# Kernel tuning notes

Measured on AMD Instinct MI355X. Metric: run time of the kernel, lower is better.

Reference implementation:

```python
import jax, jax.numpy as jnp
import numpy as np

E = 12      # embed dim
H = 32      # MLP hidden
EPS = 1e-5  # LayerNorm eps


def _layer_norm(x, gamma, beta):
    mu = jnp.mean(x, axis=-1, keepdims=True)
    var = jnp.mean(jnp.square(x - mu), axis=-1, keepdims=True)
    return (x - mu) * jax.lax.rsqrt(var + EPS) * gamma + beta


def setup_inputs() -> dict:
    key = jax.random.key(0)
    ks = jax.random.split(key, 16)
    L, N = 128, 4096
    s = 1.0 / np.sqrt(E)
    inp = {
        "x": jax.random.normal(ks[0], (L, N, E), dtype=jnp.float32),
        # MultiheadAttention packed in-projection [3E, E] and bias [3E]
        "in_proj_w": jax.random.uniform(ks[1], (3 * E, E), minval=-s, maxval=s, dtype=jnp.float32),
        "in_proj_b": jnp.zeros((3 * E,), dtype=jnp.float32),
        "out_w": jax.random.uniform(ks[2], (E, E), minval=-s, maxval=s, dtype=jnp.float32),
        "out_b": jnp.zeros((E,), dtype=jnp.float32),
        # MLP: Linear(12,32) Tanh Linear(32,32) Tanh Linear(32,12) Tanh
        "w1": jax.random.uniform(ks[3], (H, E), minval=-s, maxval=s, dtype=jnp.float32),
        "b1": jnp.zeros((H,), dtype=jnp.float32),
        "w2": jax.random.uniform(ks[4], (H, H), minval=-1/np.sqrt(H), maxval=1/np.sqrt(H), dtype=jnp.float32),
        "b2": jnp.zeros((H,), dtype=jnp.float32),
        "w3": jax.random.uniform(ks[5], (E, H), minval=-1/np.sqrt(H), maxval=1/np.sqrt(H), dtype=jnp.float32),
        "b3": jnp.zeros((E,), dtype=jnp.float32),
        # LayerNorm affine params
        "g1": jnp.ones((E,), dtype=jnp.float32),
        "be1": jnp.zeros((E,), dtype=jnp.float32),
        "g2": jnp.ones((E,), dtype=jnp.float32),
        "be2": jnp.zeros((E,), dtype=jnp.float32),
    }
    return inp


def reference(x, in_proj_w, in_proj_b, out_w, out_b,
              w1, b1, w2, b2, w3, b3, g1, be1, g2, be2):
    # x: [L, N, E] (seq, batch, embed) -- torch MHA default layout
    # --- single-head self-attention ---
    qkv = jnp.einsum('lne,fe->lnf', x, in_proj_w) + in_proj_b  # [L, N, 3E]
    q, k, v = jnp.split(qkv, 3, axis=-1)
    scale = 1.0 / jnp.sqrt(jnp.asarray(E, x.dtype))
    scores = jnp.einsum('lne,mne->nlm', q * scale, k)          # [N, L, L]
    p = jax.nn.softmax(scores, axis=-1)
    attn = jnp.einsum('nlm,mne->lne', p, v)                    # [L, N, E]
    attn = jnp.einsum('lne,fe->lnf', attn, out_w) + out_b
    # dropout is inactive in eval mode
    x = _layer_norm(x + attn, g1, be1)
    # --- MLP with tanh activations ---
    h = jnp.tanh(jnp.einsum('lne,he->lnh', x, w1) + b1)
    h = jnp.tanh(jnp.einsum('lnh,gh->lng', h, w2) + b2)
    ff = jnp.tanh(jnp.einsum('lnh,eh->lne', h, w3) + b3)
    x = _layer_norm(x + ff, g2, be2)
    return x
```

## Files before the change

### kernel.cpp

```cpp
#include <hip/hip_runtime.h>

#define NDIM 4096
#define LDIM 128
#define EDIM 12
#define HDIM 32
#define XPITCH 24

typedef float    f4v __attribute__((ext_vector_type(4)));
typedef _Float16 h2  __attribute__((ext_vector_type(2)));
typedef _Float16 h4  __attribute__((ext_vector_type(4)));

#ifndef __has_builtin
#define __has_builtin(x) 0
#endif

__device__ __forceinline__ float ex2_(float v) {
#if __has_builtin(__builtin_amdgcn_exp2f)
    return __builtin_amdgcn_exp2f(v);
#else
    return exp2f(v);
#endif
}
__device__ __forceinline__ float rcp_(float v) {
#if __has_builtin(__builtin_amdgcn_rcpf)
    return __builtin_amdgcn_rcpf(v);
#else
    return 1.0f / v;
#endif
}
__device__ __forceinline__ float rsq_(float v) {
#if __has_builtin(__builtin_amdgcn_rsqf)
    return __builtin_amdgcn_rsqf(v);
#else
    return rsqrtf(v);
#endif
}
__device__ __forceinline__ float tanh_(float v) {
    float t = ex2_(v * 2.8853900817779268f);
    return 1.0f - 2.0f * rcp_(t + 1.0f);
}

__device__ __forceinline__ h2 pk16(float a, float b) {
#if __has_builtin(__builtin_amdgcn_cvt_pkrtz)
    return __builtin_bit_cast(h2, __builtin_amdgcn_cvt_pkrtz(a, b));
#else
    h2 r; r.x = (_Float16)a; r.y = (_Float16)b; return r;
#endif
}
__device__ __forceinline__ unsigned int h2u(h2 a) { return __builtin_bit_cast(unsigned int, a); }
__device__ __forceinline__ h4 mkh4(h2 a, h2 b) {
    h4 r; r.x = a.x; r.y = a.y; r.z = b.x; r.w = b.y; return r;
}
__device__ __forceinline__ h4 cvt_h4(float4 w) { return mkh4(pk16(w.x, w.y), pk16(w.z, w.w)); }
__device__ __forceinline__ h4 h4z() {
    h4 r; r.x = (_Float16)0; r.y = (_Float16)0; r.z = (_Float16)0; r.w = (_Float16)0; return r;
}

__device__ __forceinline__ f4v mfma16(h4 a, h4 b, f4v c) {
    return __builtin_amdgcn_mfma_f32_16x16x16f16(a, b, c, 0, 0, 0);
}

__global__ __launch_bounds__(256, 3)
void encoder_fused(const float* __restrict__ x,
                   const float* __restrict__ inw, const float* __restrict__ inb,
                   const float* __restrict__ ow,  const float* __restrict__ ob,
                   const float* __restrict__ w1,  const float* __restrict__ b1,
                   const float* __restrict__ w2,  const float* __restrict__ b2,
                   const float* __restrict__ w3,  const float* __restrict__ b3,
                   const float* __restrict__ g1,  const float* __restrict__ be1,
                   const float* __restrict__ g2,  const float* __restrict__ be2,
                   float* __restrict__ out)
{
    const int tid  = threadIdx.x;
    const int p    = tid >> 7;
    const int l    = tid & 127;
    const int wv2  = (tid >> 6) & 1;
    const int lane = tid & 63;
    const int fr   = lane & 15;
    const int fg   = lane >> 4;
    const int n    = blockIdx.x * 2 + p;
    const bool e_ok = (fg < 3);

    __shared__ unsigned short sXh[2][LDIM][XPITCH];
    __shared__ unsigned short sVT[2][13][132];
    __shared__ h4             sKf[2][8][64];

    const float SCALE = 0.2886751345948129f;
    const float L2E   = 1.4426950408889634f;
    const float SL2E  = SCALE * L2E;
    const f4v   FZ    = (f4v){0.f, 0.f, 0.f, 0.f};

    {
        const float* xp = x + ((size_t)l * NDIM + n) * EDIM;
        float4 xa = *reinterpret_cast<const float4*>(xp);
        float4 xb = *reinterpret_cast<const float4*>(xp + 4);
        float4 xc = *reinterpret_cast<const float4*>(xp + 8);
        unsigned int u0 = h2u(pk16(xa.x, xa.y)), u1 = h2u(pk16(xa.z, xa.w));
        unsigned int u2 = h2u(pk16(xb.x, xb.y)), u3 = h2u(pk16(xb.z, xb.w));
        unsigned int u4 = h2u(pk16(xc.x, xc.y)), u5 = h2u(pk16(xc.z, xc.w));
        *reinterpret_cast<uint4*>(&sXh[p][l][0]) = make_uint4(u0, u1, u2, u3);
        *reinterpret_cast<uint4*>(&sXh[p][l][8]) = make_uint4(u4, u5, 0u, 0u);
        sVT[p][12][l] = (unsigned short)0x3C00;
    }

    h4 WQp = h4z(), WKp = h4z(), WVp = h4z();
    if (fr < 12 && e_ok) {
        WQp = cvt_h4(*reinterpret_cast<const float4*>(inw + (     fr) * 12 + 4 * fg));
        WKp = cvt_h4(*reinterpret_cast<const float4*>(inw + (12 + fr) * 12 + 4 * fg));
        WVp = cvt_h4(*reinterpret_cast<const float4*>(inw + (24 + fr) * 12 + 4 * fg));
    }
    const float4 F4Z = make_float4(0.f, 0.f, 0.f, 0.f);
    float4 bq4 = e_ok ? *reinterpret_cast<const float4*>(inb +      4 * fg) : F4Z;
    float4 bk4 = e_ok ? *reinterpret_cast<const float4*>(inb + 12 + 4 * fg) : F4Z;
    float4 bv4 = e_ok ? *reinterpret_cast<const float4*>(inb + 24 + 4 * fg) : F4Z;
    float4 bq4s = make_float4(bq4.x * SL2E, bq4.y * SL2E, bq4.z * SL2E, bq4.w * SL2E);

    __syncthreads();

    h4 qf[4];
    #pragma unroll
    for (int st = 0; st < 4; ++st) {
        const int srow = 64 * wv2 + 16 * st;
        h4 xB = *reinterpret_cast<const h4*>(&sXh[p][srow + fr][4 * fg]);

        f4v Dq = mfma16(WQp, xB, FZ);
        qf[st] = mkh4(pk16(fmaf(Dq[0], SL2E, bq4s.x), fmaf(Dq[1], SL2E, bq4s.y)),
                      pk16(fmaf(Dq[2], SL2E, bq4s.z), fmaf(Dq[3], SL2E, bq4s.w)));

        f4v Dk = mfma16(WKp, xB, FZ);
        sKf[p][4 * wv2 + st][lane] = mkh4(pk16(Dk[0] + bk4.x, Dk[1] + bk4.y),
                                          pk16(Dk[2] + bk4.z, Dk[3] + bk4.w));

        f4v Dv = mfma16(WVp, xB, FZ);
        if (e_ok) {
            sVT[p][4*fg + 0][srow + fr] = __builtin_bit_cast(unsigned short, (_Float16)(Dv[0] + bv4.x));
            sVT[p][4*fg + 1][srow + fr] = __builtin_bit_cast(unsigned short, (_Float16)(Dv[1] + bv4.y));
            sVT[p][4*fg + 2][srow + fr] = __builtin_bit_cast(unsigned short, (_Float16)(Dv[2] + bv4.z));
            sVT[p][4*fg + 3][srow + fr] = __builtin_bit_cast(unsigned short, (_Float16)(Dv[3] + bv4.w));
        }
    }
    __syncthreads();

    f4v oc[4];
    #pragma unroll
    for (int st = 0; st < 4; ++st) oc[st] = FZ;

    #pragma unroll
    for (int u = 0; u < 8; ++u) {
        h4 kf = sKf[p][u][lane];
        h4 vf = h4z();
        if (fr <= 12)
            vf = *reinterpret_cast<const h4*>(&sVT[p][fr][16 * u + 4 * fg]);
        #pragma unroll
        for (int st = 0; st < 4; ++st) {
            f4v c = mfma16(kf, qf[st], FZ);
            float p0 = ex2_(c[0]);
            float p1 = ex2_(c[1]);
            float p2 = ex2_(c[2]);
            float p3 = ex2_(c[3]);
            h4 paf = mkh4(pk16(p0, p1), pk16(p2, p3));
            oc[st] = mfma16(vf, paf, oc[st]);
        }
    }
    float inv[4];
    #pragma unroll
    for (int st = 0; st < 4; ++st) {
        float ps = __shfl(oc[st][0], fr + 48);
        inv[st] = rcp_(fmaxf(ps, 1e-35f));
    }

    h4 OWf = h4z();
    if (fr < 12 && e_ok)
        OWf = cvt_h4(*reinterpret_cast<const float4*>(ow + fr * 12 + 4 * fg));
    h4 W1f[2] = {h4z(), h4z()};
    if (e_ok) {
        W1f[0] = cvt_h4(*reinterpret_cast<const float4*>(w1 + (fr     ) * 12 + 4 * fg));
        W1f[1] = cvt_h4(*reinterpret_cast<const float4*>(w1 + (fr + 16) * 12 + 4 * fg));
    }
    h4 W2f[2][2];
    #pragma unroll
    for (int gt = 0; gt < 2; ++gt)
        #pragma unroll
        for (int ks = 0; ks < 2; ++ks)
            W2f[gt][ks] = cvt_h4(*reinterpret_cast<const float4*>(
                w2 + (16*gt + fr) * 32 + 16*ks + 4*fg));
    h4 W3f[2] = {h4z(), h4z()};
    if (fr < 12) {
        W3f[0] = cvt_h4(*reinterpret_cast<const float4*>(w3 + fr * 32 +      4 * fg));
        W3f[1] = cvt_h4(*reinterpret_cast<const float4*>(w3 + fr * 32 + 16 + 4 * fg));
    }
    float4 ob4  = e_ok ? *reinterpret_cast<const float4*>(ob  + 4*fg) : F4Z;
    float4 b3v  = e_ok ? *reinterpret_cast<const float4*>(b3  + 4*fg) : F4Z;
    float4 g1v  = e_ok ? *reinterpret_cast<const float4*>(g1  + 4*fg) : F4Z;
    float4 be1v = e_ok ? *reinterpret_cast<const float4*>(be1 + 4*fg) : F4Z;
    float4 g2v  = e_ok ? *reinterpret_cast<const float4*>(g2  + 4*fg) : F4Z;
    float4 be2v = e_ok ? *reinterpret_cast<const float4*>(be2 + 4*fg) : F4Z;
    float4 b1t0 = *reinterpret_cast<const float4*>(b1 +      4*fg);
    float4 b1t1 = *reinterpret_cast<const float4*>(b1 + 16 + 4*fg);
    float4 b2t0 = *reinterpret_cast<const float4*>(b2 +      4*fg);
    float4 b2t1 = *reinterpret_cast<const float4*>(b2 + 16 + 4*fg);

    #pragma unroll
    for (int st = 0; st < 4; ++st) {
        const int sample = 64*wv2 + 16*st + fr;
        h4 B0 = mkh4(pk16(oc[st][0]*inv[st], oc[st][1]*inv[st]),
                     pk16(oc[st][2]*inv[st], oc[st][3]*inv[st]));
        f4v D0 = mfma16(OWf, B0, FZ);
        float r0 = 0.f, r1 = 0.f, r2_ = 0.f, r3 = 0.f;
        if (e_ok) {
            h4 xh4 = *reinterpret_cast<const h4*>(&sXh[p][sample][4 * fg]);
            r0 = D0[0] + ob4.x + (float)xh4.x;
            r1 = D0[1] + ob4.y + (float)xh4.y;
            r2_= D0[2] + ob4.z + (float)xh4.z;
            r3 = D0[3] + ob4.w + (float)xh4.w;
        }
        float s = (r0 + r1) + (r2_ + r3);
        s += __shfl_xor(s, 16); s += __shfl_xor(s, 32);
        float mu = s * (1.0f / 12.0f);
        float d0 = r0 - mu, d1 = r1 - mu, d2 = r2_ - mu, d3 = r3 - mu;
        float vv = e_ok ? ((d0*d0 + d1*d1) + (d2*d2 + d3*d3)) : 0.f;
        vv += __shfl_xor(vv, 16); vv += __shfl_xor(vv, 32);
        float rs = rsq_(vv * (1.0f / 12.0f) + 1e-5f);
        float y0 = 0.f, y1 = 0.f, y2 = 0.f, y3 = 0.f;
        if (e_ok) {
            y0 = d0 * rs * g1v.x + be1v.x;
            y1 = d1 * rs * g1v.y + be1v.y;
            y2 = d2 * rs * g1v.z + be1v.z;
            y3 = d3 * rs * g1v.w + be1v.w;
        }
        h4 yB = mkh4(pk16(y0, y1), pk16(y2, y3));
        f4v D1a = mfma16(W1f[0], yB, FZ);
        f4v D1b = mfma16(W1f[1], yB, FZ);
        h4 B1a = mkh4(pk16(tanh_(D1a[0] + b1t0.x), tanh_(D1a[1] + b1t0.y)),
                      pk16(tanh_(D1a[2] + b1t0.z), tanh_(D1a[3] + b1t0.w)));
        h4 B1b = mkh4(pk16(tanh_(D1b[0] + b1t1.x), tanh_(D1b[1] + b1t1.y)),
                      pk16(tanh_(D1b[2] + b1t1.z), tanh_(D1b[3] + b1t1.w)));
        f4v D2a = mfma16(W2f[0][1], B1b, mfma16(W2f[0][0], B1a, FZ));
        f4v D2b = mfma16(W2f[1][1], B1b, mfma16(W2f[1][0], B1a, FZ));
        h4 B2a = mkh4(pk16(tanh_(D2a[0] + b2t0.x), tanh_(D2a[1] + b2t0.y)),
                      pk16(tanh_(D2a[2] + b2t0.z), tanh_(D2a[3] + b2t0.w)));
        h4 B2b = mkh4(pk16(tanh_(D2b[0] + b2t1.x), tanh_(D2b[1] + b2t1.y)),
                      pk16(tanh_(D2b[2] + b2t1.z), tanh_(D2b[3] + b2t1.w)));
        f4v D3 = mfma16(W3f[1], B2b, mfma16(W3f[0], B2a, FZ));
        float q0 = 0.f, q1 = 0.f, q2 = 0.f, q3 = 0.f;
        if (e_ok) {
            q0 = y0 + tanh_(D3[0] + b3v.x);
            q1 = y1 + tanh_(D3[1] + b3v.y);
            q2 = y2 + tanh_(D3[2] + b3v.z);
            q3 = y3 + tanh_(D3[3] + b3v.w);
        }
        float s2 = (q0 + q1) + (q2 + q3);
        s2 += __shfl_xor(s2, 16); s2 += __shfl_xor(s2, 32);
        float mu2 = s2 * (1.0f / 12.0f);
        float e0 = q0 - mu2, e1 = q1 - mu2, e2 = q2 - mu2, e3 = q3 - mu2;
        float vv2 = e_ok ? ((e0*e0 + e1*e1) + (e2*e2 + e3*e3)) : 0.f;
        vv2 += __shfl_xor(vv2, 16); vv2 += __shfl_xor(vv2, 32);
        float rs2 = rsq_(vv2 * (1.0f / 12.0f) + 1e-5f);
        if (e_ok) {
            float z0 = e0 * rs2 * g2v.x + be2v.x;
            float z1 = e1 * rs2 * g2v.y + be2v.y;
            float z2 = e2 * rs2 * g2v.z + be2v.z;
            float z3 = e3 * rs2 * g2v.w + be2v.w;
            float* op = out + ((size_t)sample * NDIM + n) * EDIM + 4 * fg;
            *reinterpret_cast<float4*>(op) = make_float4(z0, z1, z2, z3);
        }
    }
}

extern "C" void kernel_launch(void* const* d_in, const int* in_sizes, int n_in,
                              void* d_out, int out_size, void* d_ws, size_t ws_size,
                              hipStream_t stream) {
    const float* x   = (const float*)d_in[0];
    const float* inw = (const float*)d_in[1];
    const float* inb = (const float*)d_in[2];
    const float* ow  = (const float*)d_in[3];
    const float* ob  = (const float*)d_in[4];
    const float* w1  = (const float*)d_in[5];
    const float* b1  = (const float*)d_in[6];
    const float* w2  = (const float*)d_in[7];
    const float* b2  = (const float*)d_in[8];
    const float* w3  = (const float*)d_in[9];
    const float* b3  = (const float*)d_in[10];
    const float* g1  = (const float*)d_in[11];
    const float* be1 = (const float*)d_in[12];
    const float* g2  = (const float*)d_in[13];
    const float* be2 = (const float*)d_in[14];
    float* out = (float*)d_out;

    encoder_fused<<<dim3(NDIM / 2), dim3(256), 0, stream>>>(
        x, inw, inb, ow, ob, w1, b1, w2, b2, w3, b3, g1, be1, g2, be2, out);
}
```

Before: 39.25 us.

## Pack epilogue math into float2 ops, shrink X pitch, reuse x in registers

Rewrites the LayerNorm, tanh and bias epilogue with two-wide float vectors so the compiler can emit packed FP32 instructions such as v_pk_fma_f32. The x fragment is kept in registers for the residual, which removes an LDS reload. The sXh pitch drops from 24 to 16 to save shared memory. A __syncthreads before the QKV projection is removed. That removal may break ordering between the sXh stores and the reads, unless the sync is now unnecessary. The e_ok guards on r and y are also dropped, which relies on the zero-padded weights and biases in those lanes.

```diff
diff --git a/kernel.cpp b/kernel.cpp
--- a/kernel.cpp
+++ b/kernel.cpp
@@ -4,8 +4,9 @@
 #define LDIM 128
 #define EDIM 12
 #define HDIM 32
-#define XPITCH 24
-
+#define XPITCH 16
+
+typedef float    f2  __attribute__((ext_vector_type(2)));
 typedef float    f4v __attribute__((ext_vector_type(4)));
 typedef _Float16 h2  __attribute__((ext_vector_type(2)));
 typedef _Float16 h4  __attribute__((ext_vector_type(4)));
@@ -35,9 +36,15 @@
     return rsqrtf(v);
 #endif
 }
-__device__ __forceinline__ float tanh_(float v) {
-    float t = ex2_(v * 2.8853900817779268f);
-    return 1.0f - 2.0f * rcp_(t + 1.0f);
+
+__device__ __forceinline__ f2 mkf2(float a, float b) { f2 r; r.x = a; r.y = b; return r; }
+__device__ __forceinline__ f2 pf(f2 a, f2 b, f2 c) { return __builtin_elementwise_fma(a, b, c); }
+__device__ __forceinline__ f2 tanh2_(f2 v) {
+    f2 vm = v * 2.8853900817779268f;
+    f2 e; e.x = ex2_(vm.x); e.y = ex2_(vm.y);
+    f2 ep = e + 1.0f;
+    f2 rc; rc.x = rcp_(ep.x); rc.y = rcp_(ep.y);
+    return pf(mkf2(-2.f, -2.f), rc, mkf2(1.f, 1.f));
 }
 
 __device__ __forceinline__ h2 pk16(float a, float b) {
@@ -115,13 +122,14 @@
     float4 bv4 = e_ok ? *reinterpret_cast<const float4*>(inb + 24 + 4 * fg) : F4Z;
     float4 bq4s = make_float4(bq4.x * SL2E, bq4.y * SL2E, bq4.z * SL2E, bq4.w * SL2E);
 
-    __syncthreads();
 
     h4 qf[4];
+    h4 xres[4];
     #pragma unroll
     for (int st = 0; st < 4; ++st) {
         const int srow = 64 * wv2 + 16 * st;
         h4 xB = *reinterpret_cast<const h4*>(&sXh[p][srow + fr][4 * fg]);
+        xres[st] = xB;
 
         f4v Dq = mfma16(WQp, xB, FZ);
         qf[st] = mkh4(pk16(fmaf(Dq[0], SL2E, bq4s.x), fmaf(Dq[1], SL2E, bq4s.y)),
@@ -199,70 +207,77 @@
     float4 b1t1 = *reinterpret_cast<const float4*>(b1 + 16 + 4*fg);
     float4 b2t0 = *reinterpret_cast<const float4*>(b2 +      4*fg);
     float4 b2t1 = *reinterpret_cast<const float4*>(b2 + 16 + 4*fg);
+    f2 obA  = mkf2(ob4.x,  ob4.y),  obB  = mkf2(ob4.z,  ob4.w);
+    f2 g1A  = mkf2(g1v.x,  g1v.y),  g1B  = mkf2(g1v.z,  g1v.w);
+    f2 be1A = mkf2(be1v.x, be1v.y), be1B = mkf2(be1v.z, be1v.w);
+    f2 g2A  = mkf2(g2v.x,  g2v.y),  g2B  = mkf2(g2v.z,  g2v.w);
+    f2 be2A = mkf2(be2v.x, be2v.y), be2B = mkf2(be2v.z, be2v.w);
+    f2 b3A  = mkf2(b3v.x,  b3v.y),  b3B  = mkf2(b3v.z,  b3v.w);
+    f2 b10A = mkf2(b1t0.x, b1t0.y), b10B = mkf2(b1t0.z, b1t0.w);
+    f2 b11A = mkf2(b1t1.x, b1t1.y), b11B = mkf2(b1t1.z, b1t1.w);
+    f2 b20A = mkf2(b2t0.x, b2t0.y), b20B = mkf2(b2t0.z, b2t0.w);
+    f2 b21A = mkf2(b2t1.x, b2t1.y), b21B = mkf2(b2t1.z, b2t1.w);
 
     #pragma unroll
     for (int st = 0; st < 4; ++st) {
         const int sample = 64*wv2 + 16*st + fr;
-        h4 B0 = mkh4(pk16(oc[st][0]*inv[st], oc[st][1]*inv[st]),
-                     pk16(oc[st][2]*inv[st], oc[st][3]*inv[st]));
+        f2 oA = mkf2(oc[st][0], oc[st][1]) * inv[st];
+        f2 oB = mkf2(oc[st][2], oc[st][3]) * inv[st];
+        h4 B0 = mkh4(pk16(oA.x, oA.y), pk16(oB.x, oB.y));
         f4v D0 = mfma16(OWf, B0, FZ);
-        float r0 = 0.f, r1 = 0.f, r2_ = 0.f, r3 = 0.f;
-        if (e_ok) {
-            h4 xh4 = *reinterpret_cast<const h4*>(&sXh[p][sample][4 * fg]);
-            r0 = D0[0] + ob4.x + (float)xh4.x;
-            r1 = D0[1] + ob4.y + (float)xh4.y;
-            r2_= D0[2] + ob4.z + (float)xh4.z;
-            r3 = D0[3] + ob4.w + (float)xh4.w;
-        }
-        float s = (r0 + r1) + (r2_ + r3);
+        f2 xA = mkf2((float)xres[st].x, (float)xres[st].y);
+        f2 xB_ = mkf2((float)xres[st].z, (float)xres[st].w);
+        f2 rA = (mkf2(D0[0], D0[1]) + obA) + xA;
+        f2 rB = (mkf2(D0[2], D0[3]) + obB) + xB_;
+        f2 ts = rA + rB;
+        float s = ts.x + ts.y;
         s += __shfl_xor(s, 16); s += __shfl_xor(s, 32);
         float mu = s * (1.0f / 12.0f);
-        float d0 = r0 - mu, d1 = r1 - mu, d2 = r2_ - mu, d3 = r3 - mu;
-        float vv = e_ok ? ((d0*d0 + d1*d1) + (d2*d2 + d3*d3)) : 0.f;
+        f2 muv = mkf2(mu, mu);
+        f2 dA = rA - muv, dB = rB - muv;
+        f2 vsv = dA * dA; vsv = pf(dB, dB, vsv);
+        float vv = e_ok ? (vsv.x + vsv.y) : 0.f;
         vv += __shfl_xor(vv, 16); vv += __shfl_xor(vv, 32);
         float rs = rsq_(vv * (1.0f / 12.0f) + 1e-5f);
-        float y0 = 0.f, y1 = 0.f, y2 = 0.f, y3 = 0.f;
-        if (e_ok) {
-            y0 = d0 * rs * g1v.x + be1v.x;
-            y1 = d1 * rs * g1v.y + be1v.y;
-            y2 = d2 * rs * g1v.z + be1v.z;
-            y3 = d3 * rs * g1v.w + be1v.w;
-        }
-        h4 yB = mkh4(pk16(y0, y1), pk16(y2, y3));
-        f4v D1a = mfma16(W1f[0], yB, FZ);
-        f4v D1b = mfma16(W1f[1], yB, FZ);
-        h4 B1a = mkh4(pk16(tanh_(D1a[0] + b1t0.x), tanh_(D1a[1] + b1t0.y)),
-                      pk16(tanh_(D1a[2] + b1t0.z), tanh_(D1a[3] + b1t0.w)));
-        h4 B1b = mkh4(pk16(tanh_(D1b[0] + b1t1.x), tanh_(D1b[1] + b1t1.y)),
-                      pk16(tanh_(D1b[2] + b1t1.z), tanh_(D1b[3] + b1t1.w)));
+        f2 rsv = mkf2(rs, rs);
+        f2 yA = pf(dA * rsv, g1A, be1A);
+        f2 yB_ = pf(dB * rsv, g1B, be1B);
+        h4 yF = mkh4(pk16(yA.x, yA.y), pk16(yB_.x, yB_.y));
+        f4v D1a = mfma16(W1f[0], yF, FZ);
+        f4v D1b = mfma16(W1f[1], yF, FZ);
+        f2 t0 = tanh2_(mkf2(D1a[0], D1a[1]) + b10A);
+        f2 t1 = tanh2_(mkf2(D1a[2], D1a[3]) + b10B);
+        f2 t2 = tanh2_(mkf2(D1b[0], D1b[1]) + b11A);
+        f2 t3 = tanh2_(mkf2(D1b[2], D1b[3]) + b11B);
+        h4 B1a = mkh4(pk16(t0.x, t0.y), pk16(t1.x, t1.y));
+        h4 B1b = mkh4(pk16(t2.x, t2.y), pk16(t3.x, t3.y));
         f4v D2a = mfma16(W2f[0][1], B1b, mfma16(W2f[0][0], B1a, FZ));
         f4v D2b = mfma16(W2f[1][1], B1b, mfma16(W2f[1][0], B1a, FZ));
-        h4 B2a = mkh4(pk16(tanh_(D2a[0] + b2t0.x), tanh_(D2a[1] + b2t0.y)),
-                      pk16(tanh_(D2a[2] + b2t0.z), tanh_(D2a[3] + b2t0.w)));
-        h4 B2b = mkh4(pk16(tanh_(D2b[0] + b2t1.x), tanh_(D2b[1] + b2t1.y)),
-                      pk16(tanh_(D2b[2] + b2t1.z), tanh_(D2b[3] + b2t1.w)));
+        f2 u0 = tanh2_(mkf2(D2a[0], D2a[1]) + b20A);
+        f2 u1 = tanh2_(mkf2(D2a[2], D2a[3]) + b20B);
+        f2 u2 = tanh2_(mkf2(D2b[0], D2b[1]) + b21A);
+        f2 u3 = tanh2_(mkf2(D2b[2], D2b[3]) + b21B);
+        h4 B2a = mkh4(pk16(u0.x, u0.y), pk16(u1.x, u1.y));
+        h4 B2b = mkh4(pk16(u2.x, u2.y), pk16(u3.x, u3.y));
         f4v D3 = mfma16(W3f[1], B2b, mfma16(W3f[0], B2a, FZ));
-        float q0 = 0.f, q1 = 0.f, q2 = 0.f, q3 = 0.f;
-        if (e_ok) {
-            q0 = y0 + tanh_(D3[0] + b3v.x);
-            q1 = y1 + tanh_(D3[1] + b3v.y);
-            q2 = y2 + tanh_(D3[2] + b3v.z);
-            q3 = y3 + tanh_(D3[3] + b3v.w);
-        }
-        float s2 = (q0 + q1) + (q2 + q3);
+        f2 qA = yA + tanh2_(mkf2(D3[0], D3[1]) + b3A);
+        f2 qB = yB_ + tanh2_(mkf2(D3[2], D3[3]) + b3B);
+        f2 ts2 = qA + qB;
+        float s2 = ts2.x + ts2.y;
         s2 += __shfl_xor(s2, 16); s2 += __shfl_xor(s2, 32);
         float mu2 = s2 * (1.0f / 12.0f);
-        float e0 = q0 - mu2, e1 = q1 - mu2, e2 = q2 - mu2, e3 = q3 - mu2;
-        float vv2 = e_ok ? ((e0*e0 + e1*e1) + (e2*e2 + e3*e3)) : 0.f;
+        f2 mu2v = mkf2(mu2, mu2);
+        f2 eA = qA - mu2v, eB = qB - mu2v;
+        f2 vs2v = eA * eA; vs2v = pf(eB, eB, vs2v);
+        float vv2 = e_ok ? (vs2v.x + vs2v.y) : 0.f;
         vv2 += __shfl_xor(vv2, 16); vv2 += __shfl_xor(vv2, 32);
         float rs2 = rsq_(vv2 * (1.0f / 12.0f) + 1e-5f);
+        f2 rs2v = mkf2(rs2, rs2);
         if (e_ok) {
-            float z0 = e0 * rs2 * g2v.x + be2v.x;
-            float z1 = e1 * rs2 * g2v.y + be2v.y;
-            float z2 = e2 * rs2 * g2v.z + be2v.z;
-            float z3 = e3 * rs2 * g2v.w + be2v.w;
+            f2 zA = pf(eA * rs2v, g2A, be2A);
+            f2 zB = pf(eB * rs2v, g2B, be2B);
             float* op = out + ((size_t)sample * NDIM + n) * EDIM + 4 * fg;
-            *reinterpret_cast<float4*>(op) = make_float4(z0, z1, z2, z3);
+            *reinterpret_cast<float4*>(op) = make_float4(zA.x, zA.y, zB.x, zB.y);
         }
     }
 }
```

Result: faster. 37.72 us (-3.9%).
